# Kernel tuning notes

Measured on AMD Instinct MI355X. Metric: run time of the kernel, lower is better.

The kernel has to match this reference:

```python
import jax, jax.numpy as jnp
import numpy as np

N = 100000   # local subgraph nodes
E = 600000   # directed edges
D = 128      # memory_dim
B = 10000    # label nodes queried
C = 32       # num_classes


def _glorot(key, shape):
    s = 1.0 / np.sqrt(shape[0])
    return jax.random.uniform(key, shape, jnp.float32, -s, s)


def setup_inputs() -> dict:
    key = jax.random.key(0)
    ks = jax.random.split(key, 16)
    return {
        "node_state": jax.random.normal(ks[0], (N, D), jnp.float32),
        "edge_index": jax.random.randint(ks[1], (2, E), 0, N),
        "label_pos": jax.random.randint(ks[2], (B,), 0, N),
        # SAGEConv 1: lin_l (neighbor, with bias), lin_r (root, no bias)
        "W1l": _glorot(ks[3], (D, D)), "b1l": jnp.zeros((D,), jnp.float32),
        "W1r": _glorot(ks[4], (D, D)),
        # SAGEConv 2
        "W2l": _glorot(ks[5], (D, D)), "b2l": jnp.zeros((D,), jnp.float32),
        "W2r": _glorot(ks[6], (D, D)),
        # classifier: Linear(D,D) -> ReLU -> Linear(D,C)
        "Wc1": _glorot(ks[7], (D, D)), "bc1": jnp.zeros((D,), jnp.float32),
        "Wc2": _glorot(ks[8], (D, C)), "bc2": jnp.zeros((C,), jnp.float32),
    }


def _sage(x, src, dst, Wl, bl, Wr):
    # PyG SAGEConv, aggr='mean': out_i = lin_l(mean_{j: (j->i)} x_j) + lin_r(x_i)
    n = x.shape[0]
    agg = jax.ops.segment_sum(x[src], dst, num_segments=n)          # [N, D]
    cnt = jax.ops.segment_sum(jnp.ones_like(dst, x.dtype), dst, num_segments=n)
    mean = agg / jnp.maximum(cnt, 1.0)[:, None]
    return mean @ Wl + bl + x @ Wr


def reference(node_state, edge_index, label_pos,
              W1l, b1l, W1r, W2l, b2l, W2r, Wc1, bc1, Wc2, bc2):
    src, dst = edge_index[0], edge_index[1]
    x = jax.nn.relu(_sage(node_state, src, dst, W1l, b1l, W1r))
    x = jax.nn.relu(_sage(x, src, dst, W2l, b2l, W2r))
    h = jax.nn.relu(x[label_pos] @ Wc1 + bc1)                        # [B, D]
    return h @ Wc2 + bc2                                             # [B, C]
```

## Files before the change

### kernel.cpp

```cpp
#include <hip/hip_runtime.h>
#include <hip/hip_bf16.h>

static constexpr int N = 100000;
static constexpr int E = 600000;
static constexpr int D = 128;
static constexpr int B = 10000;
static constexpr int C = 32;

typedef __attribute__((ext_vector_type(8))) short short8;
typedef __attribute__((ext_vector_type(4))) float f32x4;

static __device__ __forceinline__ unsigned short f2bf(float f) {
    unsigned u = __float_as_uint(f);
    unsigned r = (u + 0x7FFFu + ((u >> 16) & 1u)) >> 16;
    return (unsigned short)r;
}
static __device__ __forceinline__ float bf2f(unsigned short h) {
    return __uint_as_float(((unsigned)h) << 16);
}

static __device__ __forceinline__ void split8(const float4 v0, const float4 v1,
                                              short8& h, short8& l) {
    const float f[8] = {v0.x, v0.y, v0.z, v0.w, v1.x, v1.y, v1.z, v1.w};
    #pragma unroll
    for (int i = 0; i < 8; ++i) {
        unsigned short hh = f2bf(f[i]);
        h[i] = (short)hh;
        l[i] = (short)f2bf(f[i] - bf2f(hh));
    }
}


__global__ void deg_k(const int* __restrict__ dst, int* __restrict__ deg, int nE) {
    int i = blockIdx.x * blockDim.x + threadIdx.x;
    if (i < nE) atomicAdd(&deg[dst[i]], 1);
}

__global__ __launch_bounds__(256) void scan1_k(const int* __restrict__ v,
                                               int* __restrict__ bsum, int n) {
    __shared__ int lsum[256];
    const int t = threadIdx.x;
    const int base = blockIdx.x * 1024 + t * 4;
    int s = 0;
    #pragma unroll
    for (int i = 0; i < 4; ++i) {
        int idx = base + i;
        if (idx < n) s += v[idx];
    }
    lsum[t] = s;
    __syncthreads();
    for (int off = 128; off > 0; off >>= 1) {
        if (t < off) lsum[t] += lsum[t + off];
        __syncthreads();
    }
    if (t == 0) bsum[blockIdx.x] = lsum[0];
}

__global__ __launch_bounds__(128) void scan2_k(const int* __restrict__ bsum,
                                               int* __restrict__ boff,
                                               int* __restrict__ total, int nb) {
    __shared__ int s[128];
    const int t = threadIdx.x;
    const int v = (t < nb) ? bsum[t] : 0;
    s[t] = v;
    __syncthreads();
    for (int off = 1; off < 128; off <<= 1) {
        int u = (t >= off) ? s[t - off] : 0;
        __syncthreads();
        s[t] += u;
        __syncthreads();
    }
    if (t < nb) boff[t] = s[t] - v;
    if (t == 127) *total = s[127];
}

__global__ __launch_bounds__(256) void scan3_k(const int* __restrict__ deg,
                                               const int* __restrict__ boff,
                                               int* __restrict__ roff,
                                               int* __restrict__ cur, int n) {
    __shared__ int lsum[256];
    const int t = threadIdx.x;
    const int base = blockIdx.x * 1024 + t * 4;
    int d[4];
    int s = 0;
    #pragma unroll
    for (int i = 0; i < 4; ++i) {
        int idx = base + i;
        d[i] = (idx < n) ? deg[idx] : 0;
        s += d[i];
    }
    lsum[t] = s;
    __syncthreads();
    for (int off = 1; off < 256; off <<= 1) {
        int u = (t >= off) ? lsum[t - off] : 0;
        __syncthreads();
        lsum[t] += u;
        __syncthreads();
    }
    int run = boff[blockIdx.x] + lsum[t] - s;
    #pragma unroll
    for (int i = 0; i < 4; ++i) {
        int idx = base + i;
        if (idx < n) {
            roff[idx] = run;
            cur[idx]  = run;
            run += d[i];
        }
    }
}

__global__ void fill_k(const int* __restrict__ src, const int* __restrict__ dst,
                       int* __restrict__ cur, int* __restrict__ csr_src, int nE) {
    int e = blockIdx.x * blockDim.x + threadIdx.x;
    if (e < nE) {
        int p = atomicAdd(&cur[dst[e]], 1);
        csr_src[p] = src[e];
    }
}

__global__ __launch_bounds__(256) void mark_k(
    const int* __restrict__ label_pos, const int* __restrict__ roff,
    const int* __restrict__ csr_src, int* __restrict__ flag, int nlab) {
    const int w = blockIdx.x * (blockDim.x >> 6) + (threadIdx.x >> 6);
    if (w >= nlab) return;
    const int lane = threadIdx.x & 63;
    const int v = label_pos[w];
    if (lane == 0) flag[v] = 1;
    const int jb = roff[v], je = roff[v + 1];
    for (int j = jb + lane; j < je; j += 64) flag[csr_src[j]] = 1;
}

__global__ __launch_bounds__(256) void uscan3_k(const int* __restrict__ flag,
                                                const int* __restrict__ boff,
                                                int* __restrict__ map,
                                                int* __restrict__ ulist, int n) {
    __shared__ int lsum[256];
    const int t = threadIdx.x;
    const int base = blockIdx.x * 1024 + t * 4;
    int f[4];
    int s = 0;
    #pragma unroll
    for (int i = 0; i < 4; ++i) {
        int idx = base + i;
        f[i] = (idx < n) ? flag[idx] : 0;
        s += f[i];
    }
    lsum[t] = s;
    __syncthreads();
    for (int off = 1; off < 256; off <<= 1) {
        int u = (t >= off) ? lsum[t - off] : 0;
        __syncthreads();
        lsum[t] += u;
        __syncthreads();
    }
    int run = boff[blockIdx.x] + lsum[t] - s;
    #pragma unroll
    for (int i = 0; i < 4; ++i) {
        int idx = base + i;
        if (idx < n && f[i]) {
            map[idx] = run;
            ulist[run] = idx;
            ++run;
        }
    }
}

__global__ __launch_bounds__(256) void swz_k(const float* W0, const float* W1,
                                             const float* W2, const float* W3,
                                             unsigned short* __restrict__ out) {
    const int m = blockIdx.x >> 4;
    const int chunk = blockIdx.x & 15;
    const float* W = (m == 0) ? W0 : (m == 1) ? W1 : (m == 2) ? W2 : W3;
    unsigned short* o = out + (size_t)m * 32768;
    #pragma unroll
    for (int it = 0; it < 4; ++it) {
        int f = chunk * 1024 + it * 256 + threadIdx.x;
        int j = f & 7;
        int lane = (f >> 3) & 63;
        int fi = f >> 9;
        int k = (fi >> 3) * 32 + (lane >> 4) * 8 + j;
        int n = (fi & 7) * 16 + (lane & 15);
        float a = W[k * 128 + n];
        unsigned short h = f2bf(a);
        unsigned short l = f2bf(a - bf2f(h));
        o[f] = h;
        o[16384 + f] = l;
    }
}

template <bool GATHER, bool MAP>
__global__ __launch_bounds__(256) void gather_mean_k(
    const float* __restrict__ x, const int* __restrict__ roff,
    const int* __restrict__ csr_src, const int* __restrict__ rows,
    const int* __restrict__ map, const int* __restrict__ nrows_ptr,
    float* __restrict__ out, int nrows_max) {
    const int nrows = nrows_ptr ? nrows_ptr[0] : nrows_max;
    const int w = blockIdx.x * (blockDim.x >> 6) + (threadIdx.x >> 6);
    if (w >= nrows) return;
    const int lane = threadIdx.x & 63;
    const int n  = GATHER ? rows[w] : w;
    const int jb = roff[n];
    const int je = roff[n + 1];
    const float* xb = x + lane * 2;

    float ax = 0.f, ay = 0.f;
    int j = jb;
    for (; j + 4 <= je; j += 4) {
        int s0 = csr_src[j + 0];
        int s1 = csr_src[j + 1];
        int s2 = csr_src[j + 2];
        int s3 = csr_src[j + 3];
        if (MAP) { s0 = map[s0]; s1 = map[s1]; s2 = map[s2]; s3 = map[s3]; }
        float2 v0 = *reinterpret_cast<const float2*>(xb + (size_t)s0 * D);
        float2 v1 = *reinterpret_cast<const float2*>(xb + (size_t)s1 * D);
        float2 v2 = *reinterpret_cast<const float2*>(xb + (size_t)s2 * D);
        float2 v3 = *reinterpret_cast<const float2*>(xb + (size_t)s3 * D);
        ax += v0.x + v1.x + v2.x + v3.x;
        ay += v0.y + v1.y + v2.y + v3.y;
    }
    for (; j < je; ++j) {
        int s = csr_src[j];
        if (MAP) s = map[s];
        float2 v = *reinterpret_cast<const float2*>(xb + (size_t)s * D);
        ax += v.x;
        ay += v.y;
    }
    const float inv = 1.0f / fmaxf((float)(je - jb), 1.0f);
    *reinterpret_cast<float2*>(out + (size_t)w * D + lane * 2) =
        make_float2(ax * inv, ay * inv);
}

template <bool GATHER, bool MAP>
__global__ __launch_bounds__(256, 4) void sage_mfma_k(
    const float* __restrict__ mean, const float* __restrict__ xsrc,
    const int* __restrict__ rows, const int* __restrict__ map,
    const int* __restrict__ nrows_ptr,
    const unsigned short* __restrict__ WlSw, const unsigned short* __restrict__ WrSw,
    const float* __restrict__ bl, float* __restrict__ xout, int nrows_max)
{
    const int nrows = nrows_ptr ? nrows_ptr[0] : nrows_max;
    const int rb = blockIdx.x * 64;
    if (rb >= nrows) return;

    const int t = threadIdx.x;
    const int w = t >> 6;
    const int lane = t & 63;
    const int mcol = lane & 15;
    const int q = lane >> 4;
    const int r = rb + w * 16 + mcol;

    f32x4 acc[8];
    #pragma unroll
    for (int no = 0; no < 8; ++no) acc[no] = (f32x4){0.f, 0.f, 0.f, 0.f};

    size_t gidx = 0;
    if (r < nrows) {
        int g = GATHER ? rows[r] : r;
        if (MAP) g = map[g];
        gidx = (size_t)g;
    }

    #pragma unroll
    for (int br = 0; br < 2; ++br) {
        const unsigned short* __restrict__ Wm = br ? WrSw : WlSw;
        #pragma unroll
        for (int kp = 0; kp < 4; ++kp) {
            short8 aH, aL;
            {
                float4 v0 = make_float4(0.f, 0.f, 0.f, 0.f);
                float4 v1 = make_float4(0.f, 0.f, 0.f, 0.f);
                if (r < nrows) {
                    const float* p = (br == 0)
                        ? mean + (size_t)r * D + kp * 32 + q * 8
                        : xsrc + gidx * D + kp * 32 + q * 8;
                    v0 = *reinterpret_cast<const float4*>(p);
                    v1 = *reinterpret_cast<const float4*>(p + 4);
                }
                split8(v0, v1, aH, aL);
            }
            #pragma unroll
            for (int no = 0; no < 8; ++no) {
                const size_t fo = ((size_t)(kp * 8 + no) * 64 + lane) * 8;
                short8 bh = *reinterpret_cast<const short8*>(Wm + fo);
                short8 bo = *reinterpret_cast<const short8*>(Wm + 16384 + fo);
                acc[no] = __builtin_amdgcn_mfma_f32_16x16x32_bf16(aH, bh, acc[no], 0, 0, 0);
                acc[no] = __builtin_amdgcn_mfma_f32_16x16x32_bf16(aL, bh, acc[no], 0, 0, 0);
                acc[no] = __builtin_amdgcn_mfma_f32_16x16x32_bf16(aH, bo, acc[no], 0, 0, 0);
            }
        }
    }

    #pragma unroll
    for (int no = 0; no < 8; ++no) {
        const int col = no * 16 + mcol;
        const float bias = bl[col];
        #pragma unroll
        for (int ri = 0; ri < 4; ++ri) {
            const int row = rb + w * 16 + q * 4 + ri;
            if (row < nrows)
                xout[(size_t)row * D + col] = fmaxf(acc[no][ri] + bias, 0.f);
        }
    }
}

__global__ __launch_bounds__(256) void classifier_k(
    const float* __restrict__ x2g,
    const float* __restrict__ Wc1, const float* __restrict__ bc1,
    const float* __restrict__ Wc2, const float* __restrict__ bc2,
    float* __restrict__ out, int nrows) {
    __shared__ float Xs[32][128];
    __shared__ float Hs[32][128];
    const int rb = blockIdx.x * 32;
    const int t  = threadIdx.x;

    #pragma unroll
    for (int it = 0; it < 4; ++it) {
        int j  = t + it * 256;
        int r  = j >> 5;
        int k4 = j & 31;
        int row = rb + r;
        float4 v = make_float4(0.f, 0.f, 0.f, 0.f);
        if (row < nrows) v = *reinterpret_cast<const float4*>(x2g + (size_t)row * D + k4 * 4);
        *reinterpret_cast<float4*>(&Xs[r][k4 * 4]) = v;
    }
    __syncthreads();

    {
        const int col  = t & 127;
        const int half = t >> 7;
        float acc[16];
        const float bias = bc1[col];
        #pragma unroll
        for (int i = 0; i < 16; ++i) acc[i] = bias;
        for (int k = 0; k < 128; ++k) {
            float w = Wc1[k * 128 + col];
            #pragma unroll
            for (int i = 0; i < 16; ++i)
                acc[i] = fmaf(Xs[half * 16 + i][k], w, acc[i]);
        }
        #pragma unroll
        for (int i = 0; i < 16; ++i)
            Hs[half * 16 + i][col] = fmaxf(acc[i], 0.0f);
    }
    __syncthreads();

    {
        const int c  = t & 31;
        const int rg = t >> 5;
        float o[4];
        const float b2 = bc2[c];
        #pragma unroll
        for (int i = 0; i < 4; ++i) o[i] = b2;
        for (int k = 0; k < 128; ++k) {
            float w = Wc2[k * 32 + c];
            #pragma unroll
            for (int i = 0; i < 4; ++i)
                o[i] = fmaf(Hs[rg + 8 * i][k], w, o[i]);
        }
        #pragma unroll
        for (int i = 0; i < 4; ++i) {
            int row = rb + rg + 8 * i;
            if (row < nrows) out[(size_t)row * C + c] = o[i];
        }
    }
}


extern "C" void kernel_launch(void* const* d_in, const int* in_sizes, int n_in,
                              void* d_out, int out_size, void* d_ws, size_t ws_size,
                              hipStream_t stream) {
    const float* node_state = (const float*)d_in[0];
    const int*   edge_index = (const int*)d_in[1];
    const int*   label_pos  = (const int*)d_in[2];
    const float* W1l = (const float*)d_in[3];
    const float* b1l = (const float*)d_in[4];
    const float* W1r = (const float*)d_in[5];
    const float* W2l = (const float*)d_in[6];
    const float* b2l = (const float*)d_in[7];
    const float* W2r = (const float*)d_in[8];
    const float* Wc1 = (const float*)d_in[9];
    const float* bc1 = (const float*)d_in[10];
    const float* Wc2 = (const float*)d_in[11];
    const float* bc2 = (const float*)d_in[12];
    float* out = (float*)d_out;

    const int* src = edge_index;
    const int* dst = edge_index + E;

    char* ws = (char*)d_ws;
    float* x1c   = (float*)ws;                    ws += sizeof(float) * (size_t)N * D;
    float* bufA  = (float*)ws;                    ws += sizeof(float) * (size_t)N * D;
    unsigned short* Wsw = (unsigned short*)ws;    ws += sizeof(unsigned short) * 4 * 32768;
    int* deg     = (int*)ws;                      ws += sizeof(int) * N;
    int* flag    = (int*)ws;                      ws += sizeof(int) * N;
    int* roff    = (int*)ws;                      ws += sizeof(int) * (N + 1);
    int* cur     = (int*)ws;                      ws += sizeof(int) * N;
    int* csr_src = (int*)ws;                      ws += sizeof(int) * E;
    int* map     = (int*)ws;                      ws += sizeof(int) * N;
    int* ulist   = (int*)ws;                      ws += sizeof(int) * N;
    int* bsum    = (int*)ws;                      ws += sizeof(int) * 128;
    int* boff    = (int*)ws;                      ws += sizeof(int) * 128;
    int* ucnt    = (int*)ws;                      ws += sizeof(int);
    float* mean1c = bufA;
    float* mean2g = bufA;
    float* x2g    = bufA + (size_t)B * D;

    const int TB = 256;
    const int NB = (N + 1023) / 1024;

    hipMemsetAsync(deg, 0, sizeof(int) * 2 * N, stream);
    deg_k<<<(E + TB - 1) / TB, TB, 0, stream>>>(dst, deg, E);
    scan1_k<<<NB, 256, 0, stream>>>(deg, bsum, N);
    scan2_k<<<1, 128, 0, stream>>>(bsum, boff, roff + N, NB);
    scan3_k<<<NB, 256, 0, stream>>>(deg, boff, roff, cur, N);
    fill_k<<<(E + TB - 1) / TB, TB, 0, stream>>>(src, dst, cur, csr_src, E);

    mark_k<<<(B + 3) / 4, TB, 0, stream>>>(label_pos, roff, csr_src, flag, B);
    scan1_k<<<NB, 256, 0, stream>>>(flag, bsum, N);
    scan2_k<<<1, 128, 0, stream>>>(bsum, boff, ucnt, NB);
    uscan3_k<<<NB, 256, 0, stream>>>(flag, boff, map, ulist, N);

    swz_k<<<64, 256, 0, stream>>>(W1l, W1r, W2l, W2r, Wsw);

    gather_mean_k<true, false><<<(N + 3) / 4, TB, 0, stream>>>(
        node_state, roff, csr_src, ulist, nullptr, ucnt, mean1c, N);
    sage_mfma_k<true, false><<<(N + 63) / 64, TB, 0, stream>>>(
        mean1c, node_state, ulist, nullptr, ucnt,
        Wsw, Wsw + 32768, b1l, x1c, N);

    gather_mean_k<true, true><<<(B + 3) / 4, TB, 0, stream>>>(
        x1c, roff, csr_src, label_pos, map, nullptr, mean2g, B);
    sage_mfma_k<true, true><<<(B + 63) / 64, TB, 0, stream>>>(
        mean2g, x1c, label_pos, map, nullptr,
        Wsw + 65536, Wsw + 98304, b2l, x2g, B);

    classifier_k<<<(B + 31) / 32, TB, 0, stream>>>(x2g, Wc1, bc1, Wc2, bc2, out, B);
}
```

Baseline: 295.5 us.

## Fuse CSR build, label marking and weight swizzle into one cooperative kernel

Replaces the memset and about eleven small preprocessing launches (degree count, scans, CSR fill, label marking, unique-node scan, weight swizzle) with a single cooperative kernel that uses grid-wide syncs between phases. Label neighbors are now marked during the degree pass by checking a flag on the destination, so marking no longer depends on the CSR being built first. The two scans (degrees and flags) share one block-sum pass and one offset pass. This is meant to remove launch gaps and the serial dependency chain, at the cost of grid.sync barriers and a fixed 1024-block grid that must be co-resident on the device.

```diff
diff --git a/kernel.cpp b/kernel.cpp
--- a/kernel.cpp
+++ b/kernel.cpp
@@ -1,11 +1,15 @@
 #include <hip/hip_runtime.h>
 #include <hip/hip_bf16.h>
+#include <hip/hip_cooperative_groups.h>
+
+namespace cg = cooperative_groups;
 
 static constexpr int N = 100000;
 static constexpr int E = 600000;
 static constexpr int D = 128;
 static constexpr int B = 10000;
 static constexpr int C = 32;
+static constexpr int NBc = (N + 1023) / 1024;
 
 typedef __attribute__((ext_vector_type(8))) short short8;
 typedef __attribute__((ext_vector_type(4))) float f32x4;
@@ -30,151 +34,29 @@
     }
 }
 
-
-__global__ void deg_k(const int* __restrict__ dst, int* __restrict__ deg, int nE) {
-    int i = blockIdx.x * blockDim.x + threadIdx.x;
-    if (i < nE) atomicAdd(&deg[dst[i]], 1);
-}
-
-__global__ __launch_bounds__(256) void scan1_k(const int* __restrict__ v,
-                                               int* __restrict__ bsum, int n) {
+__global__ __launch_bounds__(256) void prep_k(
+    const int* __restrict__ src, const int* __restrict__ dst,
+    const int* __restrict__ label_pos,
+    const float* __restrict__ W1l, const float* __restrict__ W1r,
+    const float* __restrict__ W2l, const float* __restrict__ W2r,
+    int* __restrict__ deg, int* __restrict__ flag,
+    int* __restrict__ roff, int* __restrict__ cur, int* __restrict__ csr_src,
+    int* __restrict__ map, int* __restrict__ ulist,
+    int* __restrict__ bsum, int* __restrict__ boff, int* __restrict__ ucnt,
+    unsigned short* __restrict__ Wsw)
+{
+    cg::grid_group grid = cg::this_grid();
     __shared__ int lsum[256];
     const int t = threadIdx.x;
-    const int base = blockIdx.x * 1024 + t * 4;
-    int s = 0;
-    #pragma unroll
-    for (int i = 0; i < 4; ++i) {
-        int idx = base + i;
-        if (idx < n) s += v[idx];
-    }
-    lsum[t] = s;
-    __syncthreads();
-    for (int off = 128; off > 0; off >>= 1) {
-        if (t < off) lsum[t] += lsum[t + off];
-        __syncthreads();
-    }
-    if (t == 0) bsum[blockIdx.x] = lsum[0];
-}
-
-__global__ __launch_bounds__(128) void scan2_k(const int* __restrict__ bsum,
-                                               int* __restrict__ boff,
-                                               int* __restrict__ total, int nb) {
-    __shared__ int s[128];
-    const int t = threadIdx.x;
-    const int v = (t < nb) ? bsum[t] : 0;
-    s[t] = v;
-    __syncthreads();
-    for (int off = 1; off < 128; off <<= 1) {
-        int u = (t >= off) ? s[t - off] : 0;
-        __syncthreads();
-        s[t] += u;
-        __syncthreads();
-    }
-    if (t < nb) boff[t] = s[t] - v;
-    if (t == 127) *total = s[127];
-}
-
-__global__ __launch_bounds__(256) void scan3_k(const int* __restrict__ deg,
-                                               const int* __restrict__ boff,
-                                               int* __restrict__ roff,
-                                               int* __restrict__ cur, int n) {
-    __shared__ int lsum[256];
-    const int t = threadIdx.x;
-    const int base = blockIdx.x * 1024 + t * 4;
-    int d[4];
-    int s = 0;
-    #pragma unroll
-    for (int i = 0; i < 4; ++i) {
-        int idx = base + i;
-        d[i] = (idx < n) ? deg[idx] : 0;
-        s += d[i];
-    }
-    lsum[t] = s;
-    __syncthreads();
-    for (int off = 1; off < 256; off <<= 1) {
-        int u = (t >= off) ? lsum[t - off] : 0;
-        __syncthreads();
-        lsum[t] += u;
-        __syncthreads();
-    }
-    int run = boff[blockIdx.x] + lsum[t] - s;
-    #pragma unroll
-    for (int i = 0; i < 4; ++i) {
-        int idx = base + i;
-        if (idx < n) {
-            roff[idx] = run;
-            cur[idx]  = run;
-            run += d[i];
-        }
-    }
-}
-
-__global__ void fill_k(const int* __restrict__ src, const int* __restrict__ dst,
-                       int* __restrict__ cur, int* __restrict__ csr_src, int nE) {
-    int e = blockIdx.x * blockDim.x + threadIdx.x;
-    if (e < nE) {
-        int p = atomicAdd(&cur[dst[e]], 1);
-        csr_src[p] = src[e];
-    }
-}
-
-__global__ __launch_bounds__(256) void mark_k(
-    const int* __restrict__ label_pos, const int* __restrict__ roff,
-    const int* __restrict__ csr_src, int* __restrict__ flag, int nlab) {
-    const int w = blockIdx.x * (blockDim.x >> 6) + (threadIdx.x >> 6);
-    if (w >= nlab) return;
-    const int lane = threadIdx.x & 63;
-    const int v = label_pos[w];
-    if (lane == 0) flag[v] = 1;
-    const int jb = roff[v], je = roff[v + 1];
-    for (int j = jb + lane; j < je; j += 64) flag[csr_src[j]] = 1;
-}
-
-__global__ __launch_bounds__(256) void uscan3_k(const int* __restrict__ flag,
-                                                const int* __restrict__ boff,
-                                                int* __restrict__ map,
-                                                int* __restrict__ ulist, int n) {
-    __shared__ int lsum[256];
-    const int t = threadIdx.x;
-    const int base = blockIdx.x * 1024 + t * 4;
-    int f[4];
-    int s = 0;
-    #pragma unroll
-    for (int i = 0; i < 4; ++i) {
-        int idx = base + i;
-        f[i] = (idx < n) ? flag[idx] : 0;
-        s += f[i];
-    }
-    lsum[t] = s;
-    __syncthreads();
-    for (int off = 1; off < 256; off <<= 1) {
-        int u = (t >= off) ? lsum[t - off] : 0;
-        __syncthreads();
-        lsum[t] += u;
-        __syncthreads();
-    }
-    int run = boff[blockIdx.x] + lsum[t] - s;
-    #pragma unroll
-    for (int i = 0; i < 4; ++i) {
-        int idx = base + i;
-        if (idx < n && f[i]) {
-            map[idx] = run;
-            ulist[run] = idx;
-            ++run;
-        }
-    }
-}
-
-__global__ __launch_bounds__(256) void swz_k(const float* W0, const float* W1,
-                                             const float* W2, const float* W3,
-                                             unsigned short* __restrict__ out) {
-    const int m = blockIdx.x >> 4;
-    const int chunk = blockIdx.x & 15;
-    const float* W = (m == 0) ? W0 : (m == 1) ? W1 : (m == 2) ? W2 : W3;
-    unsigned short* o = out + (size_t)m * 32768;
-    #pragma unroll
-    for (int it = 0; it < 4; ++it) {
-        int f = chunk * 1024 + it * 256 + threadIdx.x;
+    const int gtid = blockIdx.x * 256 + t;
+    const int gsz = gridDim.x * 256;
+
+    for (int i = gtid; i < N; i += gsz) { deg[i] = 0; flag[i] = 0; }
+    for (int f4 = gtid; f4 < 4 * 16384; f4 += gsz) {
+        const int m = f4 >> 14;
+        const int f = f4 & 16383;
+        const float* W = (m == 0) ? W1l : (m == 1) ? W1r : (m == 2) ? W2l : W2r;
+        unsigned short* o = Wsw + (size_t)m * 32768;
         int j = f & 7;
         int lane = (f >> 3) & 63;
         int fi = f >> 9;
@@ -182,9 +64,100 @@
         int n = (fi & 7) * 16 + (lane & 15);
         float a = W[k * 128 + n];
         unsigned short h = f2bf(a);
-        unsigned short l = f2bf(a - bf2f(h));
         o[f] = h;
-        o[16384 + f] = l;
+        o[16384 + f] = f2bf(a - bf2f(h));
+    }
+    grid.sync();
+
+    for (int i = gtid; i < B; i += gsz) flag[label_pos[i]] = 2;
+    grid.sync();
+
+    for (int e = gtid; e < E; e += gsz) {
+        int d = dst[e];
+        atomicAdd(&deg[d], 1);
+        if (flag[d] >= 2) atomicOr(&flag[src[e]], 1);
+    }
+    grid.sync();
+
+    for (int c = blockIdx.x; c < 2 * NBc; c += gridDim.x) {
+        const bool isdeg = c < NBc;
+        const int base = (isdeg ? c : c - NBc) * 1024 + t * 4;
+        int s = 0;
+        #pragma unroll
+        for (int i = 0; i < 4; ++i) {
+            int idx = base + i;
+            if (idx < N) s += isdeg ? deg[idx] : (flag[idx] != 0 ? 1 : 0);
+        }
+        lsum[t] = s;
+        __syncthreads();
+        for (int off = 128; off > 0; off >>= 1) {
+            if (t < off) lsum[t] += lsum[t + off];
+            __syncthreads();
+        }
+        if (t == 0) bsum[c] = lsum[0];
+        __syncthreads();
+    }
+    grid.sync();
+
+    if (blockIdx.x == 0) {
+        const int v = (t < 2 * NBc) ? bsum[t] : 0;
+        lsum[t] = v;
+        __syncthreads();
+        for (int off = 1; off < 256; off <<= 1) {
+            int u = (t >= off) ? lsum[t - off] : 0;
+            __syncthreads();
+            lsum[t] += u;
+            __syncthreads();
+        }
+        if (t < 2 * NBc) boff[t] = lsum[t] - v;
+        if (t == 0) roff[N] = E;
+        if (t == 2 * NBc - 1) *ucnt = lsum[t] - E;
+    }
+    grid.sync();
+
+    for (int c = blockIdx.x; c < 2 * NBc; c += gridDim.x) {
+        const bool isdeg = c < NBc;
+        const int base = (isdeg ? c : c - NBc) * 1024 + t * 4;
+        int d[4];
+        int s = 0;
+        #pragma unroll
+        for (int i = 0; i < 4; ++i) {
+            int idx = base + i;
+            d[i] = (idx < N) ? (isdeg ? deg[idx] : (flag[idx] != 0 ? 1 : 0)) : 0;
+            s += d[i];
+        }
+        lsum[t] = s;
+        __syncthreads();
+        for (int off = 1; off < 256; off <<= 1) {
+            int u = (t >= off) ? lsum[t - off] : 0;
+            __syncthreads();
+            lsum[t] += u;
+            __syncthreads();
+        }
+        int run = boff[c] + lsum[t] - s;
+        if (!isdeg) run -= E;
+        #pragma unroll
+        for (int i = 0; i < 4; ++i) {
+            int idx = base + i;
+            if (idx < N) {
+                if (isdeg) {
+                    roff[idx] = run;
+                    cur[idx]  = run;
+                    run += d[i];
+                } else if (d[i]) {
+                    map[idx] = run;
+                    ulist[run] = idx;
+                    ++run;
+                }
+            }
+        }
+        __syncthreads();
+    }
+    grid.sync();
+
+    for (int e = gtid; e < E; e += gsz) {
+        int p = atomicAdd(&cur[dst[e]], 1);
+        csr_src[p] = src[e];
     }
 }
 
@@ -398,29 +371,26 @@
     int* csr_src = (int*)ws;                      ws += sizeof(int) * E;
     int* map     = (int*)ws;                      ws += sizeof(int) * N;
     int* ulist   = (int*)ws;                      ws += sizeof(int) * N;
-    int* bsum    = (int*)ws;                      ws += sizeof(int) * 128;
-    int* boff    = (int*)ws;                      ws += sizeof(int) * 128;
+    int* bsum    = (int*)ws;                      ws += sizeof(int) * 256;
+    int* boff    = (int*)ws;                      ws += sizeof(int) * 256;
     int* ucnt    = (int*)ws;                      ws += sizeof(int);
     float* mean1c = bufA;
     float* mean2g = bufA;
     float* x2g    = bufA + (size_t)B * D;
 
     const int TB = 256;
-    const int NB = (N + 1023) / 1024;
-
-    hipMemsetAsync(deg, 0, sizeof(int) * 2 * N, stream);
-    deg_k<<<(E + TB - 1) / TB, TB, 0, stream>>>(dst, deg, E);
-    scan1_k<<<NB, 256, 0, stream>>>(deg, bsum, N);
-    scan2_k<<<1, 128, 0, stream>>>(bsum, boff, roff + N, NB);
-    scan3_k<<<NB, 256, 0, stream>>>(deg, boff, roff, cur, N);
-    fill_k<<<(E + TB - 1) / TB, TB, 0, stream>>>(src, dst, cur, csr_src, E);
-
-    mark_k<<<(B + 3) / 4, TB, 0, stream>>>(label_pos, roff, csr_src, flag, B);
-    scan1_k<<<NB, 256, 0, stream>>>(flag, bsum, N);
-    scan2_k<<<1, 128, 0, stream>>>(bsum, boff, ucnt, NB);
-    uscan3_k<<<NB, 256, 0, stream>>>(flag, boff, map, ulist, N);
-
-    swz_k<<<64, 256, 0, stream>>>(W1l, W1r, W2l, W2r, Wsw);
+
+    {
+        void* args[] = {
+            (void*)&src, (void*)&dst, (void*)&label_pos,
+            (void*)&W1l, (void*)&W1r, (void*)&W2l, (void*)&W2r,
+            (void*)&deg, (void*)&flag, (void*)&roff, (void*)&cur, (void*)&csr_src,
+            (void*)&map, (void*)&ulist, (void*)&bsum, (void*)&boff, (void*)&ucnt,
+            (void*)&Wsw
+        };
+        hipLaunchCooperativeKernel((const void*)prep_k, dim3(1024), dim3(256),
+                                   args, 0, stream);
+    }
 
     gather_mean_k<true, false><<<(N + 3) / 4, TB, 0, stream>>>(
         node_state, roff, csr_src, ulist, nullptr, ucnt, mean1c, N);
```

Result: slower. 933.0 us (+215.7%).
